# Performance work log

Hardware: AMD Instinct MI355X
Metric: run time of the kernel (lower is better)

The kernel has to match this reference:

```python
import jax, jax.numpy as jnp
import numpy as np

DIM = 1024

def setup_inputs() -> dict:
    key = jax.random.key(0)
    ks = jax.random.split(key, 7)
    s = 1.0 / np.sqrt(DIM)  # roughly match nn.Linear init scale
    return {
        "x": jax.random.normal(ks[0], (4, 2048, DIM), dtype=jnp.float32),
        "Wq": jax.random.normal(ks[1], (DIM, DIM), dtype=jnp.float32) * s,
        "bq": jax.random.normal(ks[2], (DIM,), dtype=jnp.float32) * s,
        "Wk": jax.random.normal(ks[3], (DIM, DIM), dtype=jnp.float32) * s,
        "bk": jax.random.normal(ks[4], (DIM,), dtype=jnp.float32) * s,
        "Wv": jax.random.normal(ks[5], (DIM, DIM), dtype=jnp.float32) * s,
        "bv": jax.random.normal(ks[6], (DIM,), dtype=jnp.float32) * s,
    }

def reference(x, Wq, bq, Wk, bk, Wv, bv):
    # torch Linear: y = x @ W.T + b
    C = x.shape[-1]
    scale = C ** (-0.5)
    q = jnp.einsum('bnc,dc->bnd', x, Wq) + bq
    k = jnp.einsum('bnc,dc->bnd', x, Wk) + bk
    v = jnp.einsum('bnc,dc->bnd', x, Wv) + bv
    attn = jnp.einsum('bnd,bmd->bnm', q, k) * scale  # [B,N,N]
    attn = jax.nn.softmax(attn, axis=-1)
    out = jnp.einsum('bnm,bmd->bnd', attn, v)
    return out
```

## Files before the change

### kernel.cpp

```cpp
#include <hip/hip_runtime.h>

#define SEQ  2048
#define DIM  1024
#define NTOK 8192
#define NQKV 3072
#define BK   64

typedef __attribute__((ext_vector_type(8)))  __bf16 bf16x8;
typedef __attribute__((ext_vector_type(16))) float  f32x16;

__device__ __forceinline__ unsigned short f2bf(float f) {
    unsigned int u = __float_as_uint(f);
    u += 0x7fffu + ((u >> 16) & 1u);
    return (unsigned short)(u >> 16);
}

__device__ __forceinline__ float bfu2f(unsigned int lo16) {
    return __uint_as_float(lo16 << 16);
}

__device__ __forceinline__ void load_lds_128(const unsigned short* g, unsigned short* l) {
    __builtin_amdgcn_global_load_lds(
        (const __attribute__((address_space(1))) void*)g,
        (__attribute__((address_space(3))) void*)l, 16, 0, 0);
}

template <int MODE>
__global__ __launch_bounds__(256)
void gemm_bt(const unsigned short* __restrict__ A, const unsigned short* __restrict__ B,
             void* __restrict__ Cv,
             const float* __restrict__ b0, const float* __restrict__ b1,
             const float* __restrict__ b2, unsigned short* __restrict__ vt,
             const float* __restrict__ inv_rs,
             int K, int lda, int ldb, int ldc,
             long sA, long sB, long sC, float alpha)
{
    __shared__ unsigned short As[128 * BK];
    __shared__ unsigned short Bs[128 * BK];

    const int tid  = threadIdx.x;
    const int wave = tid >> 6;
    const int lane = tid & 63;
    const int l31  = lane & 31;
    const int half = lane >> 5;

    const int m0 = blockIdx.x * 128;
    const int n0 = blockIdx.y * 128;
    const int z  = blockIdx.z;
    A += (long)z * sA;
    B += (long)z * sB;

    const int wm = (wave >> 1) * 64;
    const int wn = (wave & 1) * 64;

    f32x16 acc[2][2] = {};

    const int r0 = tid >> 3;
    const int g  = ((tid & 7) - r0) & 7;
    const unsigned short* Ag = A + (long)(m0 + r0) * lda + g * 8;
    const unsigned short* Bg = B + (long)(n0 + r0) * ldb + g * 8;
    unsigned short* Al = As + tid * 8;
    unsigned short* Bl = Bs + tid * 8;

    const unsigned short* Af[2][4];
    const unsigned short* Bf[2][4];
#pragma unroll
    for (int i = 0; i < 2; ++i) {
        const int rrA = wm + i * 32 + l31;
        const int rrB = wn + i * 32 + l31;
#pragma unroll
        for (int h = 0; h < 4; ++h) {
            const int gw = h * 2 + half;
            Af[i][h] = As + rrA * BK + (((gw + rrA) & 7) << 3);
            Bf[i][h] = Bs + rrB * BK + (((gw + rrB) & 7) << 3);
        }
    }

    for (int k0 = 0; k0 < K; k0 += BK) {
#pragma unroll
        for (int p = 0; p < 4; ++p) {
            load_lds_128(Ag + k0 + (long)(32 * p) * lda, Al + 2048 * p);
            load_lds_128(Bg + k0 + (long)(32 * p) * ldb, Bl + 2048 * p);
        }
        __syncthreads();
        bf16x8 a[2][4], b[2][4];
#pragma unroll
        for (int i = 0; i < 2; ++i)
#pragma unroll
            for (int h = 0; h < 4; ++h) {
                a[i][h] = *(const bf16x8*)Af[i][h];
                b[i][h] = *(const bf16x8*)Bf[i][h];
            }
#pragma unroll
        for (int h = 0; h < 4; ++h)
#pragma unroll
            for (int i = 0; i < 2; ++i)
#pragma unroll
                for (int j = 0; j < 2; ++j)
                    acc[i][j] = __builtin_amdgcn_mfma_f32_32x32x16_bf16(
                        a[i][h], b[j][h], acc[i][j], 0, 0, 0);
        __syncthreads();
    }

    if (MODE == 0) {
        if (n0 >= 2048) {
#pragma unroll
            for (int j = 0; j < 2; ++j) {
                const int d = n0 - 2048 + wn + j * 32 + l31;
                const float bias = b2[d];
#pragma unroll
                for (int i = 0; i < 2; ++i) {
                    const int mbase = m0 + wm + i * 32 + 4 * half;
#pragma unroll
                    for (int rq = 0; rq < 4; ++rq) {
                        const int rowi = mbase + 8 * rq;
                        const int bb = rowi >> 11;
                        const int mm = rowi & 2047;
                        ushort4 u;
                        u.x = f2bf(acc[i][j][rq * 4 + 0] + bias);
                        u.y = f2bf(acc[i][j][rq * 4 + 1] + bias);
                        u.z = f2bf(acc[i][j][rq * 4 + 2] + bias);
                        u.w = f2bf(acc[i][j][rq * 4 + 3] + bias);
                        *(ushort4*)(vt + ((long)bb * DIM + d) * SEQ + mm) = u;
                    }
                }
            }
        } else {
            unsigned short* C16 = (unsigned short*)Cv;
#pragma unroll
            for (int j = 0; j < 2; ++j) {
                const int col = n0 + wn + j * 32 + l31;
                const float* bp = (col >> 10) ? b1 : b0;
                const float bias = bp[col & 1023];
#pragma unroll
                for (int i = 0; i < 2; ++i)
#pragma unroll
                    for (int r = 0; r < 16; ++r) {
                        const int rowi = m0 + wm + i * 32 + (r & 3) + 8 * (r >> 2) + 4 * half;
                        C16[(long)rowi * ldc + col] = f2bf(acc[i][j][r] + bias);
                    }
            }
        }
    } else if (MODE == 1) {
        float* C = (float*)Cv + (long)z * sC;
        const float* ir = inv_rs + (long)z * SEQ;
#pragma unroll
        for (int i = 0; i < 2; ++i) {
            const int rbase = m0 + wm + i * 32 + 4 * half;
#pragma unroll
            for (int rq = 0; rq < 4; ++rq) {
                const float4 inv4 = *(const float4*)(ir + rbase + 8 * rq);
#pragma unroll
                for (int j = 0; j < 2; ++j) {
                    const int col = n0 + wn + j * 32 + l31;
                    C[(long)(rbase + 8 * rq + 0) * ldc + col] = acc[i][j][rq * 4 + 0] * inv4.x;
                    C[(long)(rbase + 8 * rq + 1) * ldc + col] = acc[i][j][rq * 4 + 1] * inv4.y;
                    C[(long)(rbase + 8 * rq + 2) * ldc + col] = acc[i][j][rq * 4 + 2] * inv4.z;
                    C[(long)(rbase + 8 * rq + 3) * ldc + col] = acc[i][j][rq * 4 + 3] * inv4.w;
                }
            }
        }
    } else {
        unsigned short* C16 = (unsigned short*)Cv + (long)z * sC;
#pragma unroll
        for (int j = 0; j < 2; ++j) {
            const int col = n0 + wn + j * 32 + l31;
#pragma unroll
            for (int i = 0; i < 2; ++i)
#pragma unroll
                for (int r = 0; r < 16; ++r) {
                    const int rowi = m0 + wm + i * 32 + (r & 3) + 8 * (r >> 2) + 4 * half;
                    C16[(long)rowi * ldc + col] = f2bf(__expf(acc[i][j][r] * alpha));
                }
        }
    }
}

__global__ __launch_bounds__(256)
void cvt_x(const float* __restrict__ src, unsigned short* __restrict__ dst, int n4)
{
    int i = blockIdx.x * 256 + threadIdx.x;
    if (i < n4) {
        float4 f = ((const float4*)src)[i];
        ushort4 u;
        u.x = f2bf(f.x); u.y = f2bf(f.y); u.z = f2bf(f.z); u.w = f2bf(f.w);
        ((ushort4*)dst)[i] = u;
    }
}

__global__ __launch_bounds__(256)
void cvt_w3(const float* __restrict__ Wq, const float* __restrict__ Wk,
            const float* __restrict__ Wv, unsigned short* __restrict__ dst)
{
    const int sel = blockIdx.y;
    const float* src = (sel == 0) ? Wq : ((sel == 1) ? Wk : Wv);
    const int i = blockIdx.x * 256 + threadIdx.x;
    float4 f = ((const float4*)src)[i];
    ushort4 u;
    u.x = f2bf(f.x); u.y = f2bf(f.y); u.z = f2bf(f.z); u.w = f2bf(f.w);
    ((ushort4*)(dst + (long)sel * DIM * DIM))[i] = u;
}

__global__ __launch_bounds__(256)
void rowsum_inv(const unsigned short* __restrict__ P, float* __restrict__ inv_rs)
{
    const int row  = blockIdx.x * 4 + (threadIdx.x >> 6);
    const int lane = threadIdx.x & 63;
    const unsigned short* pr = P + (long)row * SEQ;

    float s = 0.f;
#pragma unroll
    for (int it = 0; it < 4; ++it) {
        uint4 u = *(const uint4*)(pr + (it * 64 + lane) * 8);
        s += bfu2f(u.x & 0xffffu) + __uint_as_float(u.x & 0xffff0000u);
        s += bfu2f(u.y & 0xffffu) + __uint_as_float(u.y & 0xffff0000u);
        s += bfu2f(u.z & 0xffffu) + __uint_as_float(u.z & 0xffff0000u);
        s += bfu2f(u.w & 0xffffu) + __uint_as_float(u.w & 0xffff0000u);
    }
    for (int off = 32; off > 0; off >>= 1)
        s += __shfl_xor(s, off);
    if (lane == 0) inv_rs[row] = 1.0f / s;
}

extern "C" void kernel_launch(void* const* d_in, const int* in_sizes, int n_in,
                              void* d_out, int out_size, void* d_ws, size_t ws_size,
                              hipStream_t stream)
{
    const float* x  = (const float*)d_in[0];
    const float* Wq = (const float*)d_in[1];
    const float* bq = (const float*)d_in[2];
    const float* Wk = (const float*)d_in[3];
    const float* bk = (const float*)d_in[4];
    const float* Wv = (const float*)d_in[5];
    const float* bv = (const float*)d_in[6];
    float* out = (float*)d_out;

    char* ws = (char*)d_ws;
    unsigned short* xb   = (unsigned short*)ws;
    unsigned short* Wb   = (unsigned short*)(ws + 16u * 1024 * 1024);
    unsigned short* qkv  = (unsigned short*)(ws + 64u * 1024 * 1024);
    unsigned short* vt   = (unsigned short*)(ws + 112u * 1024 * 1024);
    unsigned short* P    = (unsigned short*)(ws + 128u * 1024 * 1024);
    float*          irs  = (float*)(ws + 160u * 1024 * 1024);

    const float scale = 0.03125f;
    dim3 blk(256);

    cvt_x<<<NTOK * DIM / 4 / 256, blk, 0, stream>>>(x, xb, NTOK * DIM / 4);
    cvt_w3<<<dim3(DIM * DIM / 4 / 256, 3), blk, 0, stream>>>(Wq, Wk, Wv, Wb);

    gemm_bt<0><<<dim3(NTOK / 128, NQKV / 128), blk, 0, stream>>>(
        xb, Wb, qkv, bq, bk, bv, vt, nullptr,
        DIM, DIM, DIM, NQKV, 0, 0, 0, 1.0f);

    gemm_bt<2><<<dim3(SEQ / 128, SEQ / 128, 4), blk, 0, stream>>>(
        qkv, qkv + 1024, P, nullptr, nullptr, nullptr, nullptr, nullptr,
        DIM, NQKV, NQKV, SEQ,
        (long)SEQ * NQKV, (long)SEQ * NQKV, (long)SEQ * SEQ, scale);

    rowsum_inv<<<NTOK / 4, blk, 0, stream>>>(P, irs);

    gemm_bt<1><<<dim3(SEQ / 128, DIM / 128, 4), blk, 0, stream>>>(
        P, vt, out, nullptr, nullptr, nullptr, nullptr, irs,
        SEQ, SEQ, SEQ, DIM,
        (long)SEQ * SEQ, (long)DIM * SEQ, (long)SEQ * DIM, 1.0f);
}
```

Measured before the change: 261.6 us.

## Double-buffer GEMM LDS tiles with BK=32 and fuse bf16 conversion kernels

The shared GEMM kernel now uses two LDS buffers with a K-tile of 32 instead of one buffer of 64. The global→LDS load for the next tile is issued before the MFMAs on the current tile, so memory latency can overlap with compute. The XOR swizzle on the LDS layout is dropped, which may bring back LDS bank conflicts, and the smaller K-tile doubles the number of barriers per GEMM. Separately, the x and weight fp32→bf16 conversions are merged into one launch to save a kernel launch.

```diff
diff --git a/kernel.cpp b/kernel.cpp
--- a/kernel.cpp
+++ b/kernel.cpp
@@ -4,7 +4,7 @@
 #define DIM  1024
 #define NTOK 8192
 #define NQKV 3072
-#define BK   64
+#define BK   32
 
 typedef __attribute__((ext_vector_type(8)))  __bf16 bf16x8;
 typedef __attribute__((ext_vector_type(16))) float  f32x16;
@@ -35,8 +35,8 @@
              int K, int lda, int ldb, int ldc,
              long sA, long sB, long sC, float alpha)
 {
-    __shared__ unsigned short As[128 * BK];
-    __shared__ unsigned short Bs[128 * BK];
+    __shared__ unsigned short As[2][128 * BK];
+    __shared__ unsigned short Bs[2][128 * BK];
 
     const int tid  = threadIdx.x;
     const int wave = tid >> 6;
@@ -55,44 +55,50 @@
 
     f32x16 acc[2][2] = {};
 
-    const int r0 = tid >> 3;
-    const int g  = ((tid & 7) - r0) & 7;
-    const unsigned short* Ag = A + (long)(m0 + r0) * lda + g * 8;
-    const unsigned short* Bg = B + (long)(n0 + r0) * ldb + g * 8;
-    unsigned short* Al = As + tid * 8;
-    unsigned short* Bl = Bs + tid * 8;
-
-    const unsigned short* Af[2][4];
-    const unsigned short* Bf[2][4];
-#pragma unroll
-    for (int i = 0; i < 2; ++i) {
-        const int rrA = wm + i * 32 + l31;
-        const int rrB = wn + i * 32 + l31;
-#pragma unroll
-        for (int h = 0; h < 4; ++h) {
-            const int gw = h * 2 + half;
-            Af[i][h] = As + rrA * BK + (((gw + rrA) & 7) << 3);
-            Bf[i][h] = Bs + rrB * BK + (((gw + rrB) & 7) << 3);
-        }
-    }
-
+    const int r0 = tid >> 2;
+    const int c0 = (tid & 3) << 3;
+    const unsigned short* Ag0 = A + (long)(m0 + r0) * lda + c0;
+    const unsigned short* Ag1 = A + (long)(m0 + 64 + r0) * lda + c0;
+    const unsigned short* Bg0 = B + (long)(n0 + r0) * ldb + c0;
+    const unsigned short* Bg1 = B + (long)(n0 + 64 + r0) * ldb + c0;
+    const int lo0 = tid * 8;
+    const int lo1 = (tid + 256) * 8;
+
+    int Afo[2][2], Bfo[2][2];
+#pragma unroll
+    for (int i = 0; i < 2; ++i)
+#pragma unroll
+        for (int h = 0; h < 2; ++h) {
+            Afo[i][h] = (wm + i * 32 + l31) * BK + h * 16 + half * 8;
+            Bfo[i][h] = (wn + i * 32 + l31) * BK + h * 16 + half * 8;
+        }
+
+    load_lds_128(Ag0, &As[0][lo0]);
+    load_lds_128(Ag1, &As[0][lo1]);
+    load_lds_128(Bg0, &Bs[0][lo0]);
+    load_lds_128(Bg1, &Bs[0][lo1]);
+    __syncthreads();
+
+#pragma unroll 2
     for (int k0 = 0; k0 < K; k0 += BK) {
-#pragma unroll
-        for (int p = 0; p < 4; ++p) {
-            load_lds_128(Ag + k0 + (long)(32 * p) * lda, Al + 2048 * p);
-            load_lds_128(Bg + k0 + (long)(32 * p) * ldb, Bl + 2048 * p);
-        }
-        __syncthreads();
-        bf16x8 a[2][4], b[2][4];
+        const int cur = (k0 / BK) & 1;
+        const int nxt = cur ^ 1;
+        if (k0 + BK < K) {
+            load_lds_128(Ag0 + k0 + BK, &As[nxt][lo0]);
+            load_lds_128(Ag1 + k0 + BK, &As[nxt][lo1]);
+            load_lds_128(Bg0 + k0 + BK, &Bs[nxt][lo0]);
+            load_lds_128(Bg1 + k0 + BK, &Bs[nxt][lo1]);
+        }
+        bf16x8 a[2][2], b[2][2];
 #pragma unroll
         for (int i = 0; i < 2; ++i)
 #pragma unroll
-            for (int h = 0; h < 4; ++h) {
-                a[i][h] = *(const bf16x8*)Af[i][h];
-                b[i][h] = *(const bf16x8*)Bf[i][h];
-            }
-#pragma unroll
-        for (int h = 0; h < 4; ++h)
+            for (int h = 0; h < 2; ++h) {
+                a[i][h] = *(const bf16x8*)&As[cur][Afo[i][h]];
+                b[i][h] = *(const bf16x8*)&Bs[cur][Bfo[i][h]];
+            }
+#pragma unroll
+        for (int h = 0; h < 2; ++h)
 #pragma unroll
             for (int i = 0; i < 2; ++i)
 #pragma unroll
@@ -177,28 +183,24 @@
 }
 
 __global__ __launch_bounds__(256)
-void cvt_x(const float* __restrict__ src, unsigned short* __restrict__ dst, int n4)
-{
-    int i = blockIdx.x * 256 + threadIdx.x;
-    if (i < n4) {
-        float4 f = ((const float4*)src)[i];
-        ushort4 u;
-        u.x = f2bf(f.x); u.y = f2bf(f.y); u.z = f2bf(f.z); u.w = f2bf(f.w);
-        ((ushort4*)dst)[i] = u;
-    }
-}
-
-__global__ __launch_bounds__(256)
-void cvt_w3(const float* __restrict__ Wq, const float* __restrict__ Wk,
-            const float* __restrict__ Wv, unsigned short* __restrict__ dst)
-{
-    const int sel = blockIdx.y;
-    const float* src = (sel == 0) ? Wq : ((sel == 1) ? Wk : Wv);
-    const int i = blockIdx.x * 256 + threadIdx.x;
-    float4 f = ((const float4*)src)[i];
+void cvt_all(const float* __restrict__ x, const float* __restrict__ Wq,
+             const float* __restrict__ Wk, const float* __restrict__ Wv,
+             unsigned short* __restrict__ xb, unsigned short* __restrict__ Wb)
+{
+    const long NX = (long)NTOK * DIM / 4;
+    const long NW = (long)DIM * DIM / 4;
+    long i = (long)blockIdx.x * 256 + threadIdx.x;
+    const float* src;
+    unsigned short* dst;
+    long j;
+    if (i < NX)               { src = x;  dst = xb;               j = i; }
+    else if (i < NX + NW)     { src = Wq; dst = Wb;               j = i - NX; }
+    else if (i < NX + 2 * NW) { src = Wk; dst = Wb + DIM * DIM;   j = i - NX - NW; }
+    else                      { src = Wv; dst = Wb + 2 * DIM * DIM; j = i - NX - 2 * NW; }
+    float4 f = ((const float4*)src)[j];
     ushort4 u;
     u.x = f2bf(f.x); u.y = f2bf(f.y); u.z = f2bf(f.z); u.w = f2bf(f.w);
-    ((ushort4*)(dst + (long)sel * DIM * DIM))[i] = u;
+    ((ushort4*)dst)[j] = u;
 }
 
 __global__ __launch_bounds__(256)
@@ -246,8 +248,8 @@
     const float scale = 0.03125f;
     dim3 blk(256);
 
-    cvt_x<<<NTOK * DIM / 4 / 256, blk, 0, stream>>>(x, xb, NTOK * DIM / 4);
-    cvt_w3<<<dim3(DIM * DIM / 4 / 256, 3), blk, 0, stream>>>(Wq, Wk, Wv, Wb);
+    cvt_all<<<(NTOK * DIM / 4 + 3 * DIM * DIM / 4) / 256, blk, 0, stream>>>(
+        x, Wq, Wk, Wv, xb, Wb);
 
     gemm_bt<0><<<dim3(NTOK / 128, NQKV / 128), blk, 0, stream>>>(
         xb, Wb, qkv, bq, bk, bv, vt, nullptr,
```

Result: slower. 299.2 us (+14.4%).

## Fuse softmax row-sum into QK^T epilogue, merge converts, add XCD-aware tile mapping

Applied to the files above, without the earlier changes.

The separate rowsum pass over P is removed. The QK^T GEMM epilogue now reduces each row's exp values with wave shuffles and atomically adds them into a zeroed row-sum buffer, and the PV GEMM takes the reciprocal itself. The two fp32-to-bf16 conversion kernels are merged into one launch. All GEMMs switch to a 1D grid remapped so that tiles sharing operands land on the same XCD for L2 reuse. This adds atomics and a memset, and the summation order becomes nondeterministic.

```diff
diff --git a/kernel.cpp b/kernel.cpp
--- a/kernel.cpp
+++ b/kernel.cpp
@@ -13,10 +13,6 @@
     unsigned int u = __float_as_uint(f);
     u += 0x7fffu + ((u >> 16) & 1u);
     return (unsigned short)(u >> 16);
-}
-
-__device__ __forceinline__ float bfu2f(unsigned int lo16) {
-    return __uint_as_float(lo16 << 16);
 }
 
 __device__ __forceinline__ void load_lds_128(const unsigned short* g, unsigned short* l) {
@@ -31,7 +27,7 @@
              void* __restrict__ Cv,
              const float* __restrict__ b0, const float* __restrict__ b1,
              const float* __restrict__ b2, unsigned short* __restrict__ vt,
-             const float* __restrict__ inv_rs,
+             float* __restrict__ rs,
              int K, int lda, int ldb, int ldc,
              long sA, long sB, long sC, float alpha)
 {
@@ -44,9 +40,21 @@
     const int l31  = lane & 31;
     const int half = lane >> 5;
 
-    const int m0 = blockIdx.x * 128;
-    const int n0 = blockIdx.y * 128;
-    const int z  = blockIdx.z;
+    int mt, nt, z;
+    {
+        const int id  = blockIdx.x;
+        const int xcd = id & 7;
+        const int c   = id >> 3;
+        if (MODE == 0) {
+            mt = c & 63;  nt = xcd * 3 + (c >> 6);          z = 0;
+        } else if (MODE == 2) {
+            nt = xcd * 2 + (c & 1); z = (c >> 1) & 3;       mt = c >> 3;
+        } else {
+            nt = xcd;               z = c & 3;              mt = c >> 2;
+        }
+    }
+    const int m0 = mt * 128;
+    const int n0 = nt * 128;
     A += (long)z * sA;
     B += (long)z * sB;
 
@@ -141,15 +149,36 @@
                     }
             }
         }
-    } else if (MODE == 1) {
+    } else if (MODE == 2) {
+        unsigned short* C16 = (unsigned short*)Cv + (long)z * sC;
+        float* rsz = rs + (long)z * SEQ;
+#pragma unroll
+        for (int i = 0; i < 2; ++i)
+#pragma unroll
+            for (int r = 0; r < 16; ++r) {
+                const int rowi = m0 + wm + i * 32 + (r & 3) + 8 * (r >> 2) + 4 * half;
+                const float p0 = __expf(acc[i][0][r] * alpha);
+                const float p1 = __expf(acc[i][1][r] * alpha);
+                C16[(long)rowi * ldc + n0 + wn + l31]      = f2bf(p0);
+                C16[(long)rowi * ldc + n0 + wn + 32 + l31] = f2bf(p1);
+                float v = p0 + p1;
+                v += __shfl_xor(v, 1);  v += __shfl_xor(v, 2);
+                v += __shfl_xor(v, 4);  v += __shfl_xor(v, 8);
+                v += __shfl_xor(v, 16);
+                if (l31 == 0) atomicAdd(rsz + rowi, v);
+            }
+    } else {
         float* C = (float*)Cv + (long)z * sC;
-        const float* ir = inv_rs + (long)z * SEQ;
+        const float* rsz = rs + (long)z * SEQ;
 #pragma unroll
         for (int i = 0; i < 2; ++i) {
             const int rbase = m0 + wm + i * 32 + 4 * half;
 #pragma unroll
             for (int rq = 0; rq < 4; ++rq) {
-                const float4 inv4 = *(const float4*)(ir + rbase + 8 * rq);
+                const float4 s4 = *(const float4*)(rsz + rbase + 8 * rq);
+                float4 inv4;
+                inv4.x = 1.0f / s4.x; inv4.y = 1.0f / s4.y;
+                inv4.z = 1.0f / s4.z; inv4.w = 1.0f / s4.w;
 #pragma unroll
                 for (int j = 0; j < 2; ++j) {
                     const int col = n0 + wn + j * 32 + l31;
@@ -160,66 +189,28 @@
                 }
             }
         }
-    } else {
-        unsigned short* C16 = (unsigned short*)Cv + (long)z * sC;
-#pragma unroll
-        for (int j = 0; j < 2; ++j) {
-            const int col = n0 + wn + j * 32 + l31;
-#pragma unroll
-            for (int i = 0; i < 2; ++i)
-#pragma unroll
-                for (int r = 0; r < 16; ++r) {
-                    const int rowi = m0 + wm + i * 32 + (r & 3) + 8 * (r >> 2) + 4 * half;
-                    C16[(long)rowi * ldc + col] = f2bf(__expf(acc[i][j][r] * alpha));
-                }
-        }
     }
 }
 
 __global__ __launch_bounds__(256)
-void cvt_x(const float* __restrict__ src, unsigned short* __restrict__ dst, int n4)
+void cvt_all(const float* __restrict__ x, const float* __restrict__ Wq,
+             const float* __restrict__ Wk, const float* __restrict__ Wv,
+             unsigned short* __restrict__ xb, unsigned short* __restrict__ Wb)
 {
-    int i = blockIdx.x * 256 + threadIdx.x;
-    if (i < n4) {
-        float4 f = ((const float4*)src)[i];
-        ushort4 u;
-        u.x = f2bf(f.x); u.y = f2bf(f.y); u.z = f2bf(f.z); u.w = f2bf(f.w);
-        ((ushort4*)dst)[i] = u;
-    }
-}
-
-__global__ __launch_bounds__(256)
-void cvt_w3(const float* __restrict__ Wq, const float* __restrict__ Wk,
-            const float* __restrict__ Wv, unsigned short* __restrict__ dst)
-{
-    const int sel = blockIdx.y;
-    const float* src = (sel == 0) ? Wq : ((sel == 1) ? Wk : Wv);
-    const int i = blockIdx.x * 256 + threadIdx.x;
-    float4 f = ((const float4*)src)[i];
+    const long NX = (long)NTOK * DIM / 4;
+    const long NW = (long)DIM * DIM / 4;
+    long i = (long)blockIdx.x * 256 + threadIdx.x;
+    const float* src;
+    unsigned short* dst;
+    long j;
+    if (i < NX)               { src = x;  dst = xb;                 j = i; }
+    else if (i < NX + NW)     { src = Wq; dst = Wb;                 j = i - NX; }
+    else if (i < NX + 2 * NW) { src = Wk; dst = Wb + DIM * DIM;     j = i - NX - NW; }
+    else                      { src = Wv; dst = Wb + 2 * DIM * DIM; j = i - NX - 2 * NW; }
+    float4 f = ((const float4*)src)[j];
     ushort4 u;
     u.x = f2bf(f.x); u.y = f2bf(f.y); u.z = f2bf(f.z); u.w = f2bf(f.w);
-    ((ushort4*)(dst + (long)sel * DIM * DIM))[i] = u;
-}
-
-__global__ __launch_bounds__(256)
-void rowsum_inv(const unsigned short* __restrict__ P, float* __restrict__ inv_rs)
-{
-    const int row  = blockIdx.x * 4 + (threadIdx.x >> 6);
-    const int lane = threadIdx.x & 63;
-    const unsigned short* pr = P + (long)row * SEQ;
-
-    float s = 0.f;
-#pragma unroll
-    for (int it = 0; it < 4; ++it) {
-        uint4 u = *(const uint4*)(pr + (it * 64 + lane) * 8);
-        s += bfu2f(u.x & 0xffffu) + __uint_as_float(u.x & 0xffff0000u);
-        s += bfu2f(u.y & 0xffffu) + __uint_as_float(u.y & 0xffff0000u);
-        s += bfu2f(u.z & 0xffffu) + __uint_as_float(u.z & 0xffff0000u);
-        s += bfu2f(u.w & 0xffffu) + __uint_as_float(u.w & 0xffff0000u);
-    }
-    for (int off = 32; off > 0; off >>= 1)
-        s += __shfl_xor(s, off);
-    if (lane == 0) inv_rs[row] = 1.0f / s;
+    ((ushort4*)dst)[j] = u;
 }
 
 extern "C" void kernel_launch(void* const* d_in, const int* in_sizes, int n_in,
@@ -241,27 +232,26 @@
     unsigned short* qkv  = (unsigned short*)(ws + 64u * 1024 * 1024);
     unsigned short* vt   = (unsigned short*)(ws + 112u * 1024 * 1024);
     unsigned short* P    = (unsigned short*)(ws + 128u * 1024 * 1024);
-    float*          irs  = (float*)(ws + 160u * 1024 * 1024);
+    float*          rs   = (float*)(ws + 160u * 1024 * 1024);
 
     const float scale = 0.03125f;
     dim3 blk(256);
 
-    cvt_x<<<NTOK * DIM / 4 / 256, blk, 0, stream>>>(x, xb, NTOK * DIM / 4);
-    cvt_w3<<<dim3(DIM * DIM / 4 / 256, 3), blk, 0, stream>>>(Wq, Wk, Wv, Wb);
-
-    gemm_bt<0><<<dim3(NTOK / 128, NQKV / 128), blk, 0, stream>>>(
+    cvt_all<<<(NTOK * DIM / 4 + 3 * DIM * DIM / 4) / 256, blk, 0, stream>>>(
+        x, Wq, Wk, Wv, xb, Wb);
+    hipMemsetAsync(rs, 0, 4 * SEQ * sizeof(float), stream);
+
+    gemm_bt<0><<<1536, blk, 0, stream>>>(
         xb, Wb, qkv, bq, bk, bv, vt, nullptr,
         DIM, DIM, DIM, NQKV, 0, 0, 0, 1.0f);
 
-    gemm_bt<2><<<dim3(SEQ / 128, SEQ / 128, 4), blk, 0, stream>>>(
-        qkv, qkv + 1024, P, nullptr, nullptr, nullptr, nullptr, nullptr,
+    gemm_bt<2><<<1024, blk, 0, stream>>>(
+        qkv, qkv + 1024, P, nullptr, nullptr, nullptr, nullptr, rs,
         DIM, NQKV, NQKV, SEQ,
         (long)SEQ * NQKV, (long)SEQ * NQKV, (long)SEQ * SEQ, scale);
 
-    rowsum_inv<<<NTOK / 4, blk, 0, stream>>>(P, irs);
-
-    gemm_bt<1><<<dim3(SEQ / 128, DIM / 128, 4), blk, 0, stream>>>(
-        P, vt, out, nullptr, nullptr, nullptr, nullptr, irs,
+    gemm_bt<1><<<512, blk, 0, stream>>>(
+        P, vt, out, nullptr, nullptr, nullptr, nullptr, rs,
         SEQ, SEQ, SEQ, DIM,
         (long)SEQ * SEQ, (long)DIM * SEQ, (long)SEQ * DIM, 1.0f);
 }
```

New measurement: 285.9 us. 9.3% more time.
